# Optimization experiments

Hardware: AMD Instinct MI355X
Metric: run time of the kernel (lower is better)

The kernel has to match this reference:

```python
import jax, jax.numpy as jnp
import numpy as np

B, S, D_IN = 64, 3072, 128
E, H, OUT = 64, 256, 10
K, STRIDE = 3, 3
T_OUT = (S - K) // STRIDE + 1  # 1024


def setup_inputs() -> dict:
    key = jax.random.key(0)
    ks = jax.random.split(key, 8)
    inputs = jax.random.normal(ks[0], (B, S, D_IN), dtype=jnp.float32)
    r = jnp.zeros((B, E, T_OUT), dtype=jnp.float32)
    s = 0.05
    conv_w = jax.random.normal(ks[1], (E, D_IN, K), dtype=jnp.float32) * s
    conv_b = jax.random.normal(ks[2], (E,), dtype=jnp.float32) * s
    w_ih = jax.random.normal(ks[3], (4 * H, E), dtype=jnp.float32) * s
    w_hh = jax.random.normal(ks[4], (4 * H, H), dtype=jnp.float32) * s
    b_ih = jax.random.normal(ks[5], (4 * H,), dtype=jnp.float32) * s
    b_hh = jax.random.normal(ks[6], (4 * H,), dtype=jnp.float32) * s
    lin_w = jax.random.normal(ks[7], (OUT, H), dtype=jnp.float32) * s
    lin_b = jnp.zeros((OUT,), dtype=jnp.float32)
    return {"inputs": inputs, "r": r, "batch_size": B,
            "conv_w": conv_w, "conv_b": conv_b,
            "w_ih": w_ih, "w_hh": w_hh, "b_ih": b_ih, "b_hh": b_hh,
            "lin_w": lin_w, "lin_b": lin_b}


def _forward(inputs, conv_w, conv_b, w_ih, w_hh, b_ih, b_hh, lin_w, lin_b):
    # F.normalize(inputs, dim=2): L2-normalize feature dim (eps=1e-12)
    norm = jnp.linalg.norm(inputs, axis=2, keepdims=True)
    x = inputs / jnp.maximum(norm, 1e-12)
    # permute(0,2,1): [B, D_IN, S], then Conv1d stride 3
    x = jnp.transpose(x, (0, 2, 1))
    emb = jax.lax.conv_general_dilated(
        x, conv_w, window_strides=(STRIDE,), padding='VALID',
        dimension_numbers=('NCH', 'OIH', 'NCH'))
    emb = emb + conv_b[None, :, None]
    act = jax.nn.relu(emb)                      # [B, E, T_OUT]
    xs = jnp.transpose(act, (2, 0, 1))          # [T, B, E] for scan

    def step(carry, x_t):
        h, c = carry
        gates = x_t @ w_ih.T + b_ih + h @ w_hh.T + b_hh  # [B, 4H]
        i_g, f_g, g_g, o_g = jnp.split(gates, 4, axis=1)
        c_new = jax.nn.sigmoid(f_g) * c + jax.nn.sigmoid(i_g) * jnp.tanh(g_g)
        h_new = jax.nn.sigmoid(o_g) * jnp.tanh(c_new)
        return (h_new, c_new), None

    h0 = jnp.zeros((inputs.shape[0], H), dtype=inputs.dtype)
    c0 = jnp.zeros((inputs.shape[0], H), dtype=inputs.dtype)
    (h_last, _), _ = jax.lax.scan(step, (h0, c0), xs)
    return h_last @ lin_w.T + lin_b             # [B, OUT]


def reference(inputs, r, batch_size, conv_w, conv_b, w_ih, w_hh, b_ih, b_hh, lin_w, lin_b):
    # mode='plain': r and batch_size are unused by the math
    return _forward(inputs, conv_w, conv_b, w_ih, w_hh, b_ih, b_hh, lin_w, lin_b)
```

## Files before the change

### kernel.cpp

```cpp
#include <hip/hip_runtime.h>
#include <math.h>

#define B_   64
#define S_   3072
#define DIN  128
#define E_   64
#define H_   256
#define OUT_ 10
#define T_   1024
#define NG   32
#define GB   2
#define NCH  8
#define GLINES 512
#define SLOT 168

#define ACT_BYTES   (B_*E_*T_*4)
#define HBUF_OFF    ACT_BYTES
#define HBUF_BYTES  (NG*2*GLINES*16)

typedef float f32x4 __attribute__((ext_vector_type(4)));

__device__ __forceinline__ f32x4 coh_load_f32x4(const float* p) {
  f32x4 r;
  asm volatile("global_load_dwordx4 %0, %1, off sc0 sc1\n\ts_waitcnt vmcnt(0)"
               : "=v"(r) : "v"(p) : "memory");
  return r;
}
__device__ __forceinline__ void coh_store_f32x4(float* p, f32x4 v) {
  asm volatile("global_store_dwordx4 %0, %1, off sc0 sc1" :: "v"(p), "v"(v) : "memory");
}

__device__ __forceinline__ float fast_sigmoid(float x) {
  return __builtin_amdgcn_rcpf(1.0f + __expf(-x));
}
__device__ __forceinline__ float fast_tanh(float x) {
  return 2.0f * __builtin_amdgcn_rcpf(1.0f + __expf(-2.0f * x)) - 1.0f;
}

__global__ __launch_bounds__(512, 1) void conv_kernel(
    const float* __restrict__ in,
    const float* __restrict__ cw,
    const float* __restrict__ cb,
    float* __restrict__ actT)
{
  extern __shared__ float xs[];
  float4* xs4 = (float4*)xs;
  const int bid = blockIdx.x;
  const int b  = bid >> 4;
  const int tb = bid & 15;
  const int tid = threadIdx.x;

  const float4* gin = (const float4*)(in + (size_t)b*S_*DIN + (size_t)tb*192*DIN);
  #pragma unroll
  for (int i = 0; i < 12; ++i) {
    int f4 = tid + i*512;
    int r = f4 >> 5, dq = f4 & 31;
    xs4[r*32 + (dq ^ (r & 7))] = gin[f4];
  }
  __syncthreads();

  const int wv = tid >> 6, ln = tid & 63;
  for (int rr = 0; rr < 24; ++rr) {
    int r = wv*24 + rr;
    int u = r*32 + ((ln >> 1) ^ (r & 7));
    float2* p = (float2*)((char*)xs + (size_t)u*16 + (size_t)(ln & 1)*8);
    float2 v = *p;
    float s = v.x*v.x + v.y*v.y;
    #pragma unroll
    for (int off = 32; off >= 1; off >>= 1) s += __shfl_xor(s, off);
    float inv = 1.0f / fmaxf(sqrtf(s), 1e-12f);
    v.x *= inv; v.y *= inv;
    *p = v;
  }
  __syncthreads();

  const int eo = __builtin_amdgcn_readfirstlane(wv);
  float acc[8];
  #pragma unroll
  for (int j = 0; j < 8; ++j) acc[j] = cb[eo*8 + j];

  const int r0 = 3*ln, r1 = 3*ln + 1, r2 = 3*ln + 2;
  #pragma unroll 4
  for (int dq = 0; dq < 32; ++dq) {
    float4 x0 = xs4[r0*32 + (dq ^ (r0 & 7))];
    float4 x1 = xs4[r1*32 + (dq ^ (r1 & 7))];
    float4 x2 = xs4[r2*32 + (dq ^ (r2 & 7))];
    #pragma unroll
    for (int j = 0; j < 8; ++j) {
      const float* wp = cw + (size_t)(eo*8 + j)*(DIN*3) + dq*12;
      acc[j] += x0.x*wp[0] + x1.x*wp[1] + x2.x*wp[2]
              + x0.y*wp[3] + x1.y*wp[4] + x2.y*wp[5]
              + x0.z*wp[6] + x1.z*wp[7] + x2.z*wp[8]
              + x0.w*wp[9] + x1.w*wp[10] + x2.w*wp[11];
    }
  }

  const int tg = tb*64 + ln;
  #pragma unroll
  for (int j = 0; j < 8; ++j) {
    int e = eo*8 + j;
    actT[(size_t)b*E_*T_ + (size_t)e*T_ + tg] = fmaxf(acc[j], 0.0f);
  }
}

__global__ __launch_bounds__(512, 1) void lstm_kernel(
    const float* __restrict__ actT,
    const float* __restrict__ w_ih,
    const float* __restrict__ w_hh,
    const float* __restrict__ b_ih,
    const float* __restrict__ b_hh,
    float* hbuf)
{
  __shared__ float sl[2][2][2][SLOT];

  const int bid = blockIdx.x;
  const int g = bid & 31;
  const int q = bid >> 5;
  const int tid = threadIdx.x;
  const int w = tid >> 6;
  const int l = tid & 63;

  const int khalf = l & 1;
  const int m     = (l >> 1) & 3;
  const int b     = w & 1;
  const int hh    = (w >> 1)*8 + (l >> 3);
  const int row   = m*256 + 32*q + hh;

  float4 wv[40];
  if (khalf == 0) {
    const float4* ph = (const float4*)(w_hh + (size_t)row*H_);
    #pragma unroll
    for (int i = 0; i < 40; ++i) wv[i] = ph[i];
  } else {
    const float4* ph = (const float4*)(w_hh + (size_t)row*H_) + 40;
    #pragma unroll
    for (int i = 0; i < 24; ++i) wv[i] = ph[i];
    const float4* px = (const float4*)(w_ih + (size_t)row*E_);
    #pragma unroll
    for (int i = 0; i < 16; ++i) wv[24+i] = px[i];
  }
  const float bias = (khalf == 0) ? (b_ih[row] + b_hh[row]) : 0.0f;

  for (int i = tid; i < 2*2*2*SLOT; i += 512) ((float*)sl)[i] = 0.0f;

  const int pb   = tid >> 8;
  const int pidx = tid & 255;
  const int pkh  = (pidx < 160) ? 0 : 1;
  const int pslot= (pidx < 160) ? pidx : pidx - 160;

  const int xb = ((tid - 384) >> 6) & 1, xe = tid & 63;
  const float* actp = actT + (size_t)((g*GB + xb)*E_ + xe)*T_;
  const bool is_x = (tid >= 384);

  float* hb = hbuf + (size_t)g*(2*GLINES*4);

  float c = 0.0f;
  for (int t = 0; t < T_; ++t) {
    const int p = t & 1;

    float xval = 0.0f;
    if (is_x) xval = actp[t];

    if (t > 0) {
      const float* lp = hb + (size_t)(p*GLINES + pb*256 + pidx)*4;
      f32x4 v = coh_load_f32x4(lp);
      while (__float_as_int(v[3]) != t) v = coh_load_f32x4(lp);
      sl[p][pb][pkh][pslot] = v[0];
    }
    if (is_x) sl[p][xb][1][96 + xe] = xval;
    __syncthreads();

    float acc = bias;
    {
      const float* hs = &sl[p][b][khalf][0];
      #pragma unroll
      for (int i = 0; i < 40; ++i) {
        float4 h4 = *(const float4*)(hs + i*4);
        acc += wv[i].x*h4.x + wv[i].y*h4.y + wv[i].z*h4.z + wv[i].w*h4.w;
      }
    }

    float ksum = acc + __shfl_xor(acc, 1);
    float x1 = __shfl_xor(ksum, 2);
    float x2 = __shfl_xor(ksum, 4);
    float x3 = __shfl_xor(x1, 4);
    float gi = (m==0)?ksum:(m==1)?x1 :(m==2)?x2 :x3;
    float gf = (m==0)?x1 :(m==1)?ksum:(m==2)?x3 :x2;
    float gg = (m==0)?x2 :(m==1)?x3 :(m==2)?ksum:x1;
    float go = (m==0)?x3 :(m==1)?x2 :(m==2)?x1 :ksum;

    float si = fast_sigmoid(gi);
    float sf = fast_sigmoid(gf);
    float so = fast_sigmoid(go);
    c = sf*c + si*fast_tanh(gg);
    float h = so*fast_tanh(c);

    if ((l & 7) == 0) {
      f32x4 line;
      line[0] = h; line[1] = 0.f; line[2] = 0.f;
      line[3] = __int_as_float(t + 1);
      float* dp = hb + (size_t)((((t+1) & 1)*GLINES) + b*256 + 32*q + hh)*4;
      coh_store_f32x4(dp, line);
    }
  }
}

__global__ void head_kernel(const float* __restrict__ hbuf,
                            const float* __restrict__ lw,
                            const float* __restrict__ lb,
                            float* __restrict__ out)
{
  int idx = blockIdx.x*blockDim.x + threadIdx.x;
  if (idx >= B_*OUT_) return;
  int b = idx / OUT_, o = idx % OUT_;
  int g = b >> 1, bl = b & 1;
  const float* lines = hbuf + (size_t)g*(2*GLINES*4);
  const float* wv = lw + (size_t)o*H_;
  float s = lb[o];
  #pragma unroll 8
  for (int k = 0; k < H_; ++k) s += lines[(size_t)(bl*256 + k)*4] * wv[k];
  out[idx] = s;
}

extern "C" void kernel_launch(void* const* d_in, const int* in_sizes, int n_in,
                              void* d_out, int out_size, void* d_ws, size_t ws_size,
                              hipStream_t stream) {
  const float* inputs = (const float*)d_in[0];
  const float* conv_w = (const float*)d_in[3];
  const float* conv_b = (const float*)d_in[4];
  const float* w_ih   = (const float*)d_in[5];
  const float* w_hh   = (const float*)d_in[6];
  const float* b_ih   = (const float*)d_in[7];
  const float* b_hh   = (const float*)d_in[8];
  const float* lin_w  = (const float*)d_in[9];
  const float* lin_b  = (const float*)d_in[10];

  float* actT = (float*)d_ws;
  float* hbuf = (float*)((char*)d_ws + HBUF_OFF);

  hipMemsetAsync(hbuf, 0, HBUF_BYTES, stream);
  hipLaunchKernelGGL(conv_kernel, dim3(B_*16), dim3(512), 192*128*4, stream,
                     inputs, conv_w, conv_b, actT);
  hipLaunchKernelGGL(lstm_kernel, dim3(NG*NCH), dim3(512), 0, stream,
                     actT, w_ih, w_hh, b_ih, b_hh, hbuf);
  hipLaunchKernelGGL(head_kernel, dim3(3), dim3(256), 0, stream,
                     hbuf, lin_w, lin_b, (float*)d_out);
}
```

Measured before the change: 2.415 ms.

## Pack three h values per coherent line and skip polling own chunk

Each global exchange line now carries three hidden values plus the step flag, which cuts the line count from 512 to 192 per group. Only other blocks' lines are polled, and each block writes its own h values straight into shared memory for the next step. This reduces the coherent loads and stores on the serial recurrence critical path. The final hidden state is written to a separate buffer for the head kernel. The cost is extra shuffles and fewer threads doing each poll.

```diff
diff --git a/kernel.cpp b/kernel.cpp
--- a/kernel.cpp
+++ b/kernel.cpp
@@ -11,12 +11,14 @@
 #define NG   32
 #define GB   2
 #define NCH  8
-#define GLINES 512
+#define NLINES 192
 #define SLOT 168
 
 #define ACT_BYTES   (B_*E_*T_*4)
 #define HBUF_OFF    ACT_BYTES
-#define HBUF_BYTES  (NG*2*GLINES*16)
+#define HBUF_BYTES  (NG*2*NLINES*16)
+#define HFINAL_OFF  (HBUF_OFF + HBUF_BYTES)
+#define HFINAL_BYTES (NG*GB*H_*4)
 
 typedef float f32x4 __attribute__((ext_vector_type(4)));
 
@@ -103,13 +105,19 @@
   }
 }
 
+__device__ __forceinline__ void kmap(int hidx, int& kh, int& slot) {
+  kh = (hidx < 160) ? 0 : 1;
+  slot = (hidx < 160) ? hidx : hidx - 160;
+}
+
 __global__ __launch_bounds__(512, 1) void lstm_kernel(
     const float* __restrict__ actT,
     const float* __restrict__ w_ih,
     const float* __restrict__ w_hh,
     const float* __restrict__ b_ih,
     const float* __restrict__ b_hh,
-    float* hbuf)
+    float* hbuf,
+    float* hfinal)
 {
   __shared__ float sl[2][2][2][SLOT];
 
@@ -122,8 +130,10 @@
 
   const int khalf = l & 1;
   const int m     = (l >> 1) & 3;
+  const int o     = l >> 3;
   const int b     = w & 1;
-  const int hh    = (w >> 1)*8 + (l >> 3);
+  const int wh    = w >> 1;
+  const int hh    = wh*8 + o;
   const int row   = m*256 + 32*q + hh;
 
   float4 wv[40];
@@ -143,16 +153,25 @@
 
   for (int i = tid; i < 2*2*2*SLOT; i += 512) ((float*)sl)[i] = 0.0f;
 
-  const int pb   = tid >> 8;
-  const int pidx = tid & 255;
-  const int pkh  = (pidx < 160) ? 0 : 1;
-  const int pslot= (pidx < 160) ? pidx : pidx - 160;
-
-  const int xb = ((tid - 384) >> 6) & 1, xe = tid & 63;
+  const int pq = tid / 24, pw = (tid % 24) / 3, ps = tid % 3;
+  const bool is_poll = (tid < 192) && (pq != q);
+  const int pb = pw & 1;
+  const int phh0 = 32*pq + (pw >> 1)*8 + 3*ps;
+  const int pcnt = (ps == 2) ? 2 : 3;
+
+  const bool is_x = (tid >= 384);
+  const int xi = tid - 384, xb = (xi >> 6) & 1, xe = xi & 63;
   const float* actp = actT + (size_t)((g*GB + xb)*E_ + xe)*T_;
-  const bool is_x = (tid >= 384);
-
-  float* hb = hbuf + (size_t)g*(2*GLINES*4);
+
+  const int ss = l / 24;
+  const bool is_store = ((l % 24) == 0);
+  const int sline = q*24 + w*3 + ss;
+  const int shh0 = wh*8 + 3*ss;
+  const int scnt = (ss == 2) ? 2 : 3;
+
+  float* hb = hbuf + (size_t)g*(2*NLINES*4);
+
+  __syncthreads();
 
   float c = 0.0f;
   for (int t = 0; t < T_; ++t) {
@@ -161,11 +180,17 @@
     float xval = 0.0f;
     if (is_x) xval = actp[t];
 
-    if (t > 0) {
-      const float* lp = hb + (size_t)(p*GLINES + pb*256 + pidx)*4;
+    if (t > 0 && is_poll) {
+      const float* lp = hb + (size_t)(p*NLINES + tid)*4;
       f32x4 v = coh_load_f32x4(lp);
       while (__float_as_int(v[3]) != t) v = coh_load_f32x4(lp);
-      sl[p][pb][pkh][pslot] = v[0];
+      #pragma unroll
+      for (int j = 0; j < 3; ++j) {
+        if (j < pcnt) {
+          int kh, slot; kmap(phh0 + j, kh, slot);
+          sl[p][pb][kh][slot] = v[j];
+        }
+      }
     }
     if (is_x) sl[p][xb][1][96 + xe] = xval;
     __syncthreads();
@@ -195,17 +220,33 @@
     c = sf*c + si*fast_tanh(gg);
     float h = so*fast_tanh(c);
 
-    if ((l & 7) == 0) {
+    float v1 = __shfl(h, (l + 8) & 63, 64);
+    float v2 = __shfl(h, (l + 16) & 63, 64);
+    if (is_store) {
       f32x4 line;
-      line[0] = h; line[1] = 0.f; line[2] = 0.f;
+      line[0] = h; line[1] = v1; line[2] = v2;
       line[3] = __int_as_float(t + 1);
-      float* dp = hb + (size_t)((((t+1) & 1)*GLINES) + b*256 + 32*q + hh)*4;
+      float* dp = hb + (size_t)((((t+1) & 1)*NLINES) + sline)*4;
       coh_store_f32x4(dp, line);
-    }
-  }
-}
-
-__global__ void head_kernel(const float* __restrict__ hbuf,
+      #pragma unroll
+      for (int j = 0; j < 3; ++j) {
+        if (j < scnt) {
+          int kh, slot; kmap(32*q + shh0 + j, kh, slot);
+          sl[p ^ 1][b][kh][slot] = (j == 0) ? h : (j == 1) ? v1 : v2;
+        }
+      }
+      if (t == T_ - 1) {
+        #pragma unroll
+        for (int j = 0; j < 3; ++j)
+          if (j < scnt)
+            hfinal[(size_t)g*GB*H_ + (size_t)b*H_ + 32*q + shh0 + j]
+                = (j == 0) ? h : (j == 1) ? v1 : v2;
+      }
+    }
+  }
+}
+
+__global__ void head_kernel(const float* __restrict__ hfinal,
                             const float* __restrict__ lw,
                             const float* __restrict__ lb,
                             float* __restrict__ out)
@@ -214,11 +255,11 @@
   if (idx >= B_*OUT_) return;
   int b = idx / OUT_, o = idx % OUT_;
   int g = b >> 1, bl = b & 1;
-  const float* lines = hbuf + (size_t)g*(2*GLINES*4);
+  const float* h = hfinal + (size_t)g*GB*H_ + (size_t)bl*H_;
   const float* wv = lw + (size_t)o*H_;
   float s = lb[o];
   #pragma unroll 8
-  for (int k = 0; k < H_; ++k) s += lines[(size_t)(bl*256 + k)*4] * wv[k];
+  for (int k = 0; k < H_; ++k) s += h[k]*wv[k];
   out[idx] = s;
 }
 
@@ -235,14 +276,15 @@
   const float* lin_w  = (const float*)d_in[9];
   const float* lin_b  = (const float*)d_in[10];
 
-  float* actT = (float*)d_ws;
-  float* hbuf = (float*)((char*)d_ws + HBUF_OFF);
+  float* actT   = (float*)d_ws;
+  float* hbuf   = (float*)((char*)d_ws + HBUF_OFF);
+  float* hfinal = (float*)((char*)d_ws + HFINAL_OFF);
 
   hipMemsetAsync(hbuf, 0, HBUF_BYTES, stream);
   hipLaunchKernelGGL(conv_kernel, dim3(B_*16), dim3(512), 192*128*4, stream,
                      inputs, conv_w, conv_b, actT);
   hipLaunchKernelGGL(lstm_kernel, dim3(NG*NCH), dim3(512), 0, stream,
-                     actT, w_ih, w_hh, b_ih, b_hh, hbuf);
+                     actT, w_ih, w_hh, b_ih, b_hh, hbuf, hfinal);
   hipLaunchKernelGGL(head_kernel, dim3(3), dim3(256), 0, stream,
-                     hbuf, lin_w, lin_b, (float*)d_out);
-}
+                     hfinal, lin_w, lin_b, (float*)d_out);
+}
```

After: 2.118 ms. 12.3% less time.
